# Performance work log

Measured on AMD Instinct MI355X. Metric: run time of the kernel, lower is better.

## Reference

```python
import jax, jax.numpy as jnp
import numpy as np

K = 2            # number of attention heads (k in __init__)
NEG = -9.0e15    # mask fill value from the torch code
N, C, CO = 6144, 128, 128


def _ln(x, g, b, eps=1e-5):
    m = x.mean(-1, keepdims=True)
    v = ((x - m) ** 2).mean(-1, keepdims=True)
    return (x - m) / jnp.sqrt(v + eps) * g + b


def setup_inputs() -> dict:
    key = jax.random.key(0)
    ks = jax.random.split(key, 6)
    x = jax.random.normal(ks[0], (N, C), jnp.float32)
    adj = (jax.random.uniform(ks[1], (N, N)) < 0.01).astype(jnp.float32)
    ff0_w = jax.random.normal(ks[2], (K, C, C), jnp.float32) / np.float32(np.sqrt(C))
    ff1_w = jax.random.normal(ks[3], (K, CO, C), jnp.float32) / np.float32(np.sqrt(C))
    attn_w = jax.random.normal(ks[4], (K, 2 * C), jnp.float32) / np.float32(np.sqrt(2 * C))
    return dict(
        x=x, adj=adj, ff0_w=ff0_w, ff1_w=ff1_w, attn_w=attn_w,
        g1=jnp.ones((C,), jnp.float32), b1=jnp.zeros((C,), jnp.float32),
        g2=jnp.ones((C,), jnp.float32), b2=jnp.zeros((C,), jnp.float32),
    )


def reference(x, adj, ff0_w, ff1_w, attn_w, g1, b1, g2, b2):
    n, c = x.shape
    co = ff1_w.shape[1]
    x_norm = _ln(x, g1, b1)
    # torch does adj = adj + eye(n) each iteration; since adj >= 0 the mask
    # (adj > 0) is identical for every iteration: original edges plus self-loops.
    mask = (adj > 0) | jnp.eye(n, dtype=bool)
    h_next = jnp.zeros((n, co), x.dtype)
    for i in range(K):  # small fixed head count, structurally distinct weights
        h = x_norm @ ff0_w[i].T  # [n, c]
        # attn_fc(cat(h_i, h_j)) == a1.h_i + a2.h_j  (exact decomposition of
        # the concat+linear; avoids materializing the [n, n, 2c] tensor)
        s_src = h @ attn_w[i, :c]  # [n], contribution of row node i
        s_dst = h @ attn_w[i, c:]  # [n], contribution of col node j
        e = jax.nn.leaky_relu(s_src[:, None] + s_dst[None, :])  # [n, n]
        e = jnp.where(mask, e, jnp.float32(NEG))
        atten = jax.nn.softmax(e, axis=1)  # dropout p=0.0 -> identity
        att = atten @ h + x  # residual adds pre-norm x
        att = _ln(att, g2, b2)
        h_next = h_next + jax.nn.elu(att @ ff1_w[i].T) / K
    return h_next
```

## Files before the change

### kernel.cpp

```cpp
#include <hip/hip_runtime.h>
#include <math.h>

#define Nn 6144
#define Cc 128
#define NHD 2
#define NBRS 192

__device__ __forceinline__ float wave_red_sum(float v) {
#pragma unroll
  for (int o = 32; o; o >>= 1) v += __shfl_xor(v, o);
  return v;
}

__global__ __launch_bounds__(256) void k_ln(const float* __restrict__ x,
                                            const float* __restrict__ g,
                                            const float* __restrict__ b,
                                            float* __restrict__ xn) {
  int wid = threadIdx.x >> 6, lane = threadIdx.x & 63;
  int row = blockIdx.x * 4 + wid;
  float2 v = ((const float2*)(x + (size_t)row * Cc))[lane];
  float s = v.x + v.y;
#pragma unroll
  for (int o = 32; o; o >>= 1) s += __shfl_xor(s, o);
  float mean = s * (1.0f / Cc);
  float dx = v.x - mean, dy = v.y - mean;
  float q = dx * dx + dy * dy;
#pragma unroll
  for (int o = 32; o; o >>= 1) q += __shfl_xor(q, o);
  float rstd = rsqrtf(q * (1.0f / Cc) + 1e-5f);
  int c = lane * 2;
  float* o = xn + (size_t)row * Cc;
  o[c]     = dx * rstd * g[c] + b[c];
  o[c + 1] = dy * rstd * g[c + 1] + b[c + 1];
}

template <int MODE>
__global__ __launch_bounds__(256) void k_gemm(const float* __restrict__ A,
                                              const float* __restrict__ Bw,
                                              float* __restrict__ out) {
  __shared__ float As[64][68];
  __shared__ float Bs[64][132];
  const int t = threadIdx.x;
  const int head = blockIdx.y;
  const int row0 = blockIdx.x * 64;
  const float* Ah = A + (MODE == 1 ? (size_t)head * Nn * Cc : (size_t)0);
  const float* Bh = Bw + (size_t)head * Cc * Cc;
  const int tr = t & 15, tc = t >> 4;
  const int r0 = tr * 4, c0 = tc * 8;
  float acc[4][8];
#pragma unroll
  for (int i = 0; i < 4; i++)
#pragma unroll
    for (int j = 0; j < 8; j++) acc[i][j] = 0.f;

  for (int kt = 0; kt < Cc; kt += 64) {
    __syncthreads();
    for (int i = t; i < 1024; i += 256) {
      int rr = i >> 4, k4 = i & 15;
      float4 v = *(const float4*)(Ah + (size_t)(row0 + rr) * Cc + kt + k4 * 4);
      As[k4 * 4 + 0][rr] = v.x; As[k4 * 4 + 1][rr] = v.y;
      As[k4 * 4 + 2][rr] = v.z; As[k4 * 4 + 3][rr] = v.w;
    }
    for (int i = t; i < 2048; i += 256) {
      int cc2 = i >> 4, k4 = i & 15;
      float4 v = *(const float4*)(Bh + (size_t)cc2 * Cc + kt + k4 * 4);
      Bs[k4 * 4 + 0][cc2] = v.x; Bs[k4 * 4 + 1][cc2] = v.y;
      Bs[k4 * 4 + 2][cc2] = v.z; Bs[k4 * 4 + 3][cc2] = v.w;
    }
    __syncthreads();
#pragma unroll
    for (int k = 0; k < 64; k++) {
      float4 a  = *(const float4*)&As[k][r0];
      float4 b0 = *(const float4*)&Bs[k][c0];
      float4 b1 = *(const float4*)&Bs[k][c0 + 4];
      float av[4] = {a.x, a.y, a.z, a.w};
      float bv[8] = {b0.x, b0.y, b0.z, b0.w, b1.x, b1.y, b1.z, b1.w};
#pragma unroll
      for (int i = 0; i < 4; i++)
#pragma unroll
        for (int j = 0; j < 8; j++) acc[i][j] = fmaf(av[i], bv[j], acc[i][j]);
    }
  }
#pragma unroll
  for (int i = 0; i < 4; i++) {
    float o[8];
#pragma unroll
    for (int j = 0; j < 8; j++) {
      float v = acc[i][j];
      if (MODE == 1) { v = (v > 0.f) ? v : (expf(v) - 1.f); v *= 0.5f; }
      o[j] = v;
    }
    float* op = out + ((size_t)head * Nn + row0 + r0 + i) * Cc + c0;
    *(float4*)(op)     = make_float4(o[0], o[1], o[2], o[3]);
    *(float4*)(op + 4) = make_float4(o[4], o[5], o[6], o[7]);
  }
}

__global__ __launch_bounds__(256) void k_attn_s(const float* __restrict__ h,
                                                const float* __restrict__ aw,
                                                float* __restrict__ ssrc,
                                                float* __restrict__ sdst) {
  int wid = threadIdx.x >> 6, lane = threadIdx.x & 63;
  int row = blockIdx.x * 4 + wid;
#pragma unroll
  for (int hd = 0; hd < NHD; hd++) {
    float2 v  = ((const float2*)(h + ((size_t)hd * Nn + row) * Cc))[lane];
    float2 w1 = ((const float2*)(aw + hd * 2 * Cc))[lane];
    float2 w2 = ((const float2*)(aw + hd * 2 * Cc + Cc))[lane];
    float a = v.x * w1.x + v.y * w1.y;
    float b = v.x * w2.x + v.y * w2.y;
#pragma unroll
    for (int o = 32; o; o >>= 1) { a += __shfl_xor(a, o); b += __shfl_xor(b, o); }
    if (lane == 0) { ssrc[hd * Nn + row] = a; sdst[hd * Nn + row] = b; }
  }
}

__global__ __launch_bounds__(256) void k_csr(
    const float* __restrict__ adj, const float* __restrict__ ssrc,
    const float* __restrict__ sdst, int* __restrict__ nbr,
    int* __restrict__ deg, float* __restrict__ wtsg) {
  __shared__ int nbr_s[4][NBRS];
  const int lane = threadIdx.x & 63;
  const int wid = threadIdx.x >> 6;
  const int r = blockIdx.x * 4 + wid;
  const float4* arow = (const float4*)(adj + (size_t)r * Nn);
  const unsigned long long ltmask = (1ull << lane) - 1ull;
  int cnt = 0;
  for (int i = lane; i < Nn / 4; i += 64) {
    float4 v = arow[i];
    int j = i * 4;
    bool p0 = (v.x > 0.f) || (j + 0 == r);
    bool p1 = (v.y > 0.f) || (j + 1 == r);
    bool p2 = (v.z > 0.f) || (j + 2 == r);
    bool p3 = (v.w > 0.f) || (j + 3 == r);
    unsigned long long m0 = __ballot(p0);
    unsigned long long m1 = __ballot(p1);
    unsigned long long m2 = __ballot(p2);
    unsigned long long m3 = __ballot(p3);
    int c0 = __popcll(m0), c1 = __popcll(m1), c2 = __popcll(m2), c3 = __popcll(m3);
    if (p0) nbr_s[wid][cnt + __popcll(m0 & ltmask)] = j;
    if (p1) nbr_s[wid][cnt + c0 + __popcll(m1 & ltmask)] = j + 1;
    if (p2) nbr_s[wid][cnt + c0 + c1 + __popcll(m2 & ltmask)] = j + 2;
    if (p3) nbr_s[wid][cnt + c0 + c1 + c2 + __popcll(m3 & ltmask)] = j + 3;
    cnt += c0 + c1 + c2 + c3;
  }
  if (cnt > NBRS) cnt = NBRS;
  const float s0 = ssrc[r], s1 = ssrc[Nn + r];
  float e0v[3], e1v[3];
  float m0 = -3.0e38f, m1 = -3.0e38f;
#pragma unroll
  for (int it = 0; it < 3; it++) {
    int k = it * 64 + lane;
    float a0 = -3.0e38f, a1 = -3.0e38f;
    if (k < cnt) {
      int j = nbr_s[wid][k];
      a0 = s0 + sdst[j];
      a1 = s1 + sdst[Nn + j];
      a0 = (a0 > 0.f) ? a0 : 0.01f * a0;
      a1 = (a1 > 0.f) ? a1 : 0.01f * a1;
    }
    e0v[it] = a0; e1v[it] = a1;
    m0 = fmaxf(m0, a0); m1 = fmaxf(m1, a1);
  }
#pragma unroll
  for (int o = 32; o; o >>= 1) {
    m0 = fmaxf(m0, __shfl_xor(m0, o));
    m1 = fmaxf(m1, __shfl_xor(m1, o));
  }
  float t0 = 0.f, t1 = 0.f;
  float w0v[3], w1v[3];
#pragma unroll
  for (int it = 0; it < 3; it++) {
    int k = it * 64 + lane;
    float w0 = (k < cnt) ? __expf(e0v[it] - m0) : 0.f;
    float w1 = (k < cnt) ? __expf(e1v[it] - m1) : 0.f;
    w0v[it] = w0; w1v[it] = w1; t0 += w0; t1 += w1;
  }
#pragma unroll
  for (int o = 32; o; o >>= 1) { t0 += __shfl_xor(t0, o); t1 += __shfl_xor(t1, o); }
  const float i0 = 1.0f / t0, i1 = 1.0f / t1;
  int* nrow = nbr + (size_t)r * NBRS;
  float* w0row = wtsg + (size_t)r * NBRS;
  float* w1row = wtsg + (size_t)(Nn + r) * NBRS;
#pragma unroll
  for (int it = 0; it < 3; it++) {
    int k = it * 64 + lane;
    if (k < cnt) {
      nrow[k] = nbr_s[wid][k];
      w0row[k] = w0v[it] * i0;
      w1row[k] = w1v[it] * i1;
    }
  }
  if (lane == 0) deg[r] = cnt;
}

__global__ __launch_bounds__(256) void k_gather(
    const int* __restrict__ nbr, const int* __restrict__ degp,
    const float* __restrict__ wtsg, const float* __restrict__ x,
    const float* __restrict__ h, const float* __restrict__ g2,
    const float* __restrict__ b2, float* __restrict__ att_out) {
  __shared__ int nbr_s[NBRS];
  __shared__ float wts[NHD][NBRS];
  __shared__ float red[8];
  const int t = threadIdx.x;
  const int r = blockIdx.x;
  const int deg = degp[r];
  if (t < deg) {
    nbr_s[t] = nbr[(size_t)r * NBRS + t];
    wts[0][t] = wtsg[(size_t)r * NBRS + t];
    wts[1][t] = wtsg[(size_t)(Nn + r) * NBRS + t];
  }
  __syncthreads();
  const int hd = t >> 7;
  const int c = t & 127;
  const float* hp = h + (size_t)hd * Nn * Cc + c;
  const float* wrow = wts[hd];
  float acc = 0.f;
  int k = 0;
  for (; k + 8 <= deg; k += 8) {
    int j0 = nbr_s[k],     j1 = nbr_s[k + 1], j2 = nbr_s[k + 2], j3 = nbr_s[k + 3];
    int j4 = nbr_s[k + 4], j5 = nbr_s[k + 5], j6 = nbr_s[k + 6], j7 = nbr_s[k + 7];
    float a0 = hp[(size_t)j0 * Cc], a1 = hp[(size_t)j1 * Cc];
    float a2 = hp[(size_t)j2 * Cc], a3 = hp[(size_t)j3 * Cc];
    float a4 = hp[(size_t)j4 * Cc], a5 = hp[(size_t)j5 * Cc];
    float a6 = hp[(size_t)j6 * Cc], a7 = hp[(size_t)j7 * Cc];
    acc = fmaf(wrow[k],     a0, acc); acc = fmaf(wrow[k + 1], a1, acc);
    acc = fmaf(wrow[k + 2], a2, acc); acc = fmaf(wrow[k + 3], a3, acc);
    acc = fmaf(wrow[k + 4], a4, acc); acc = fmaf(wrow[k + 5], a5, acc);
    acc = fmaf(wrow[k + 6], a6, acc); acc = fmaf(wrow[k + 7], a7, acc);
  }
  for (; k < deg; k++) acc = fmaf(wrow[k], hp[(size_t)nbr_s[k] * Cc], acc);
  float att = acc + x[(size_t)r * Cc + c];
  float s = wave_red_sum(att);
  int wid = t >> 6;
  __syncthreads();
  if ((t & 63) == 0) red[wid] = s;
  __syncthreads();
  float mean = (red[hd * 2] + red[hd * 2 + 1]) * (1.0f / Cc);
  float d = att - mean;
  float q = wave_red_sum(d * d);
  __syncthreads();
  if ((t & 63) == 0) red[wid] = q;
  __syncthreads();
  float var = (red[hd * 2] + red[hd * 2 + 1]) * (1.0f / Cc);
  float rstd = rsqrtf(var + 1e-5f);
  att_out[((size_t)hd * Nn + r) * Cc + c] = d * rstd * g2[c] + b2[c];
}

__global__ __launch_bounds__(256) void k_combine(const float* __restrict__ a,
                                                 const float* __restrict__ b,
                                                 float* __restrict__ o) {
  int i = (blockIdx.x * 256 + threadIdx.x) * 4;
  float4 va = *(const float4*)(a + i);
  float4 vb = *(const float4*)(b + i);
  *(float4*)(o + i) = make_float4(va.x + vb.x, va.y + vb.y, va.z + vb.z, va.w + vb.w);
}

extern "C" void kernel_launch(void* const* d_in, const int* in_sizes, int n_in,
                              void* d_out, int out_size, void* d_ws, size_t ws_size,
                              hipStream_t stream) {
  const float* x   = (const float*)d_in[0];
  const float* adj = (const float*)d_in[1];
  const float* ff0 = (const float*)d_in[2];
  const float* ff1 = (const float*)d_in[3];
  const float* aw  = (const float*)d_in[4];
  const float* g1  = (const float*)d_in[5];
  const float* b1  = (const float*)d_in[6];
  const float* g2  = (const float*)d_in[7];
  const float* b2  = (const float*)d_in[8];
  float* out = (float*)d_out;

  float* ws    = (float*)d_ws;
  float* xnorm = ws;
  float* h     = xnorm + (size_t)Nn * Cc;
  float* ssrc  = h + (size_t)2 * Nn * Cc;
  float* sdst  = ssrc + 2 * Nn;
  float* attn  = sdst + 2 * Nn;
  float* outh  = attn + (size_t)2 * Nn * Cc;
  float* wtsg  = outh + (size_t)2 * Nn * Cc;
  int*   nbr   = (int*)(wtsg + (size_t)2 * Nn * NBRS);
  int*   deg   = nbr + (size_t)Nn * NBRS;

  hipLaunchKernelGGL(k_ln, dim3(Nn / 4), dim3(256), 0, stream, x, g1, b1, xnorm);
  hipLaunchKernelGGL((k_gemm<0>), dim3(Nn / 64, NHD), dim3(256), 0, stream, xnorm, ff0, h);
  hipLaunchKernelGGL(k_attn_s, dim3(Nn / 4), dim3(256), 0, stream, h, aw, ssrc, sdst);
  hipLaunchKernelGGL(k_csr, dim3(Nn / 4), dim3(256), 0, stream, adj, ssrc, sdst, nbr, deg, wtsg);
  hipLaunchKernelGGL(k_gather, dim3(Nn), dim3(256), 0, stream,
                     nbr, deg, wtsg, x, h, g2, b2, attn);
  hipLaunchKernelGGL((k_gemm<1>), dim3(Nn / 64, NHD), dim3(256), 0, stream, attn, ff1, outh);
  hipLaunchKernelGGL(k_combine, dim3((Nn * Cc) / 1024), dim3(256), 0, stream,
                     outh, outh + (size_t)Nn * Cc, out);
}
```

Baseline: 312.9 us.

## Store projected features in bf16 and fuse head-sum into second GEMM

```diff
diff --git a/kernel.cpp b/kernel.cpp
--- a/kernel.cpp
+++ b/kernel.cpp
@@ -5,6 +5,18 @@
 #define Cc 128
 #define NHD 2
 #define NBRS 192
+
+typedef unsigned short u16;
+typedef unsigned int u32;
+
+__device__ __forceinline__ float bf2f(u16 u) {
+  union { u32 i; float f; } v; v.i = ((u32)u) << 16; return v.f;
+}
+__device__ __forceinline__ u16 f2bf(float f) {
+  union { float f; u32 i; } v; v.f = f;
+  u32 r = (v.i + 0x7FFFu + ((v.i >> 16) & 1u)) >> 16;
+  return (u16)r;
+}
 
 __device__ __forceinline__ float wave_red_sum(float v) {
 #pragma unroll
@@ -34,16 +46,14 @@
   o[c + 1] = dy * rstd * g[c + 1] + b[c + 1];
 }
 
-template <int MODE>
-__global__ __launch_bounds__(256) void k_gemm(const float* __restrict__ A,
-                                              const float* __restrict__ Bw,
-                                              float* __restrict__ out) {
+__global__ __launch_bounds__(256) void k_ff0(const float* __restrict__ A,
+                                             const float* __restrict__ Bw,
+                                             u16* __restrict__ hb) {
   __shared__ float As[64][68];
   __shared__ float Bs[64][132];
   const int t = threadIdx.x;
   const int head = blockIdx.y;
   const int row0 = blockIdx.x * 64;
-  const float* Ah = A + (MODE == 1 ? (size_t)head * Nn * Cc : (size_t)0);
   const float* Bh = Bw + (size_t)head * Cc * Cc;
   const int tr = t & 15, tc = t >> 4;
   const int r0 = tr * 4, c0 = tc * 8;
@@ -57,7 +67,7 @@
     __syncthreads();
     for (int i = t; i < 1024; i += 256) {
       int rr = i >> 4, k4 = i & 15;
-      float4 v = *(const float4*)(Ah + (size_t)(row0 + rr) * Cc + kt + k4 * 4);
+      float4 v = *(const float4*)(A + (size_t)(row0 + rr) * Cc + kt + k4 * 4);
       As[k4 * 4 + 0][rr] = v.x; As[k4 * 4 + 1][rr] = v.y;
       As[k4 * 4 + 2][rr] = v.z; As[k4 * 4 + 3][rr] = v.w;
     }
@@ -83,20 +93,18 @@
   }
 #pragma unroll
   for (int i = 0; i < 4; i++) {
-    float o[8];
-#pragma unroll
-    for (int j = 0; j < 8; j++) {
-      float v = acc[i][j];
-      if (MODE == 1) { v = (v > 0.f) ? v : (expf(v) - 1.f); v *= 0.5f; }
-      o[j] = v;
-    }
-    float* op = out + ((size_t)head * Nn + row0 + r0 + i) * Cc + c0;
-    *(float4*)(op)     = make_float4(o[0], o[1], o[2], o[3]);
-    *(float4*)(op + 4) = make_float4(o[4], o[5], o[6], o[7]);
-  }
-}
-
-__global__ __launch_bounds__(256) void k_attn_s(const float* __restrict__ h,
+    u16* op = hb + ((size_t)head * Nn + row0 + r0 + i) * Cc + c0;
+    ushort4 o0, o1;
+    o0.x = f2bf(acc[i][0]); o0.y = f2bf(acc[i][1]);
+    o0.z = f2bf(acc[i][2]); o0.w = f2bf(acc[i][3]);
+    o1.x = f2bf(acc[i][4]); o1.y = f2bf(acc[i][5]);
+    o1.z = f2bf(acc[i][6]); o1.w = f2bf(acc[i][7]);
+    *(ushort4*)(op)     = o0;
+    *(ushort4*)(op + 4) = o1;
+  }
+}
+
+__global__ __launch_bounds__(256) void k_attn_s(const u16* __restrict__ hb,
                                                 const float* __restrict__ aw,
                                                 float* __restrict__ ssrc,
                                                 float* __restrict__ sdst) {
@@ -104,11 +112,13 @@
   int row = blockIdx.x * 4 + wid;
 #pragma unroll
   for (int hd = 0; hd < NHD; hd++) {
-    float2 v  = ((const float2*)(h + ((size_t)hd * Nn + row) * Cc))[lane];
+    u32 packed = ((const u32*)(hb + ((size_t)hd * Nn + row) * Cc))[lane];
+    float hx = bf2f((u16)(packed & 0xFFFF));
+    float hy = bf2f((u16)(packed >> 16));
     float2 w1 = ((const float2*)(aw + hd * 2 * Cc))[lane];
     float2 w2 = ((const float2*)(aw + hd * 2 * Cc + Cc))[lane];
-    float a = v.x * w1.x + v.y * w1.y;
-    float b = v.x * w2.x + v.y * w2.y;
+    float a = hx * w1.x + hy * w1.y;
+    float b = hx * w2.x + hy * w2.y;
 #pragma unroll
     for (int o = 32; o; o >>= 1) { a += __shfl_xor(a, o); b += __shfl_xor(b, o); }
     if (lane == 0) { ssrc[hd * Nn + row] = a; sdst[hd * Nn + row] = b; }
@@ -197,7 +207,7 @@
 __global__ __launch_bounds__(256) void k_gather(
     const int* __restrict__ nbr, const int* __restrict__ degp,
     const float* __restrict__ wtsg, const float* __restrict__ x,
-    const float* __restrict__ h, const float* __restrict__ g2,
+    const u16* __restrict__ hb, const float* __restrict__ g2,
     const float* __restrict__ b2, float* __restrict__ att_out) {
   __shared__ int nbr_s[NBRS];
   __shared__ float wts[NHD][NBRS];
@@ -213,23 +223,23 @@
   __syncthreads();
   const int hd = t >> 7;
   const int c = t & 127;
-  const float* hp = h + (size_t)hd * Nn * Cc + c;
+  const u16* hp = hb + (size_t)hd * Nn * Cc + c;
   const float* wrow = wts[hd];
   float acc = 0.f;
   int k = 0;
   for (; k + 8 <= deg; k += 8) {
     int j0 = nbr_s[k],     j1 = nbr_s[k + 1], j2 = nbr_s[k + 2], j3 = nbr_s[k + 3];
     int j4 = nbr_s[k + 4], j5 = nbr_s[k + 5], j6 = nbr_s[k + 6], j7 = nbr_s[k + 7];
-    float a0 = hp[(size_t)j0 * Cc], a1 = hp[(size_t)j1 * Cc];
-    float a2 = hp[(size_t)j2 * Cc], a3 = hp[(size_t)j3 * Cc];
-    float a4 = hp[(size_t)j4 * Cc], a5 = hp[(size_t)j5 * Cc];
-    float a6 = hp[(size_t)j6 * Cc], a7 = hp[(size_t)j7 * Cc];
-    acc = fmaf(wrow[k],     a0, acc); acc = fmaf(wrow[k + 1], a1, acc);
-    acc = fmaf(wrow[k + 2], a2, acc); acc = fmaf(wrow[k + 3], a3, acc);
-    acc = fmaf(wrow[k + 4], a4, acc); acc = fmaf(wrow[k + 5], a5, acc);
-    acc = fmaf(wrow[k + 6], a6, acc); acc = fmaf(wrow[k + 7], a7, acc);
-  }
-  for (; k < deg; k++) acc = fmaf(wrow[k], hp[(size_t)nbr_s[k] * Cc], acc);
+    u16 a0 = hp[(size_t)j0 * Cc], a1 = hp[(size_t)j1 * Cc];
+    u16 a2 = hp[(size_t)j2 * Cc], a3 = hp[(size_t)j3 * Cc];
+    u16 a4 = hp[(size_t)j4 * Cc], a5 = hp[(size_t)j5 * Cc];
+    u16 a6 = hp[(size_t)j6 * Cc], a7 = hp[(size_t)j7 * Cc];
+    acc = fmaf(wrow[k],     bf2f(a0), acc); acc = fmaf(wrow[k + 1], bf2f(a1), acc);
+    acc = fmaf(wrow[k + 2], bf2f(a2), acc); acc = fmaf(wrow[k + 3], bf2f(a3), acc);
+    acc = fmaf(wrow[k + 4], bf2f(a4), acc); acc = fmaf(wrow[k + 5], bf2f(a5), acc);
+    acc = fmaf(wrow[k + 6], bf2f(a6), acc); acc = fmaf(wrow[k + 7], bf2f(a7), acc);
+  }
+  for (; k < deg; k++) acc = fmaf(wrow[k], bf2f(hp[(size_t)nbr_s[k] * Cc]), acc);
   float att = acc + x[(size_t)r * Cc + c];
   float s = wave_red_sum(att);
   int wid = t >> 6;
@@ -247,13 +257,71 @@
   att_out[((size_t)hd * Nn + r) * Cc + c] = d * rstd * g2[c] + b2[c];
 }
 
-__global__ __launch_bounds__(256) void k_combine(const float* __restrict__ a,
-                                                 const float* __restrict__ b,
-                                                 float* __restrict__ o) {
-  int i = (blockIdx.x * 256 + threadIdx.x) * 4;
-  float4 va = *(const float4*)(a + i);
-  float4 vb = *(const float4*)(b + i);
-  *(float4*)(o + i) = make_float4(va.x + vb.x, va.y + vb.y, va.z + vb.z, va.w + vb.w);
+__global__ __launch_bounds__(256) void k_ff1(const float* __restrict__ A,
+                                             const float* __restrict__ Bw,
+                                             float* __restrict__ out) {
+  __shared__ float As[64][68];
+  __shared__ float Bs[64][68];
+  const int t = threadIdx.x;
+  const int row0 = blockIdx.x * 64;
+  const int ch = blockIdx.y;
+  const int tr = t & 15, tc = t >> 4;
+  const int r0 = tr * 4, c0 = tc * 4;
+  float fin[4][4];
+#pragma unroll
+  for (int i = 0; i < 4; i++)
+#pragma unroll
+    for (int j = 0; j < 4; j++) fin[i][j] = 0.f;
+
+  for (int head = 0; head < NHD; head++) {
+    const float* Ah = A + (size_t)head * Nn * Cc;
+    const float* Bh = Bw + (size_t)head * Cc * Cc + (size_t)ch * 64 * Cc;
+    float acc[4][4];
+#pragma unroll
+    for (int i = 0; i < 4; i++)
+#pragma unroll
+      for (int j = 0; j < 4; j++) acc[i][j] = 0.f;
+    for (int kt = 0; kt < Cc; kt += 64) {
+      __syncthreads();
+      for (int i = t; i < 1024; i += 256) {
+        int rr = i >> 4, k4 = i & 15;
+        float4 v = *(const float4*)(Ah + (size_t)(row0 + rr) * Cc + kt + k4 * 4);
+        As[k4 * 4 + 0][rr] = v.x; As[k4 * 4 + 1][rr] = v.y;
+        As[k4 * 4 + 2][rr] = v.z; As[k4 * 4 + 3][rr] = v.w;
+      }
+      for (int i = t; i < 1024; i += 256) {
+        int cc2 = i >> 4, k4 = i & 15;
+        float4 v = *(const float4*)(Bh + (size_t)cc2 * Cc + kt + k4 * 4);
+        Bs[k4 * 4 + 0][cc2] = v.x; Bs[k4 * 4 + 1][cc2] = v.y;
+        Bs[k4 * 4 + 2][cc2] = v.z; Bs[k4 * 4 + 3][cc2] = v.w;
+      }
+      __syncthreads();
+#pragma unroll
+      for (int k = 0; k < 64; k++) {
+        float4 a = *(const float4*)&As[k][r0];
+        float4 b = *(const float4*)&Bs[k][c0];
+        float av[4] = {a.x, a.y, a.z, a.w};
+        float bv[4] = {b.x, b.y, b.z, b.w};
+#pragma unroll
+        for (int i = 0; i < 4; i++)
+#pragma unroll
+          for (int j = 0; j < 4; j++) acc[i][j] = fmaf(av[i], bv[j], acc[i][j]);
+      }
+    }
+#pragma unroll
+    for (int i = 0; i < 4; i++)
+#pragma unroll
+      for (int j = 0; j < 4; j++) {
+        float v = acc[i][j];
+        v = (v > 0.f) ? v : (expf(v) - 1.f);
+        fin[i][j] += 0.5f * v;
+      }
+  }
+#pragma unroll
+  for (int i = 0; i < 4; i++) {
+    float* op = out + (size_t)(row0 + r0 + i) * Cc + ch * 64 + c0;
+    *(float4*)op = make_float4(fin[i][0], fin[i][1], fin[i][2], fin[i][3]);
+  }
 }
 
 extern "C" void kernel_launch(void* const* d_in, const int* in_sizes, int n_in,
@@ -272,22 +340,19 @@
 
   float* ws    = (float*)d_ws;
   float* xnorm = ws;
-  float* h     = xnorm + (size_t)Nn * Cc;
-  float* ssrc  = h + (size_t)2 * Nn * Cc;
+  float* ssrc  = xnorm + (size_t)Nn * Cc;
   float* sdst  = ssrc + 2 * Nn;
   float* attn  = sdst + 2 * Nn;
-  float* outh  = attn + (size_t)2 * Nn * Cc;
-  float* wtsg  = outh + (size_t)2 * Nn * Cc;
+  float* wtsg  = attn + (size_t)2 * Nn * Cc;
   int*   nbr   = (int*)(wtsg + (size_t)2 * Nn * NBRS);
   int*   deg   = nbr + (size_t)Nn * NBRS;
+  u16*   hb    = (u16*)(deg + Nn);
 
   hipLaunchKernelGGL(k_ln, dim3(Nn / 4), dim3(256), 0, stream, x, g1, b1, xnorm);
-  hipLaunchKernelGGL((k_gemm<0>), dim3(Nn / 64, NHD), dim3(256), 0, stream, xnorm, ff0, h);
-  hipLaunchKernelGGL(k_attn_s, dim3(Nn / 4), dim3(256), 0, stream, h, aw, ssrc, sdst);
+  hipLaunchKernelGGL(k_ff0, dim3(Nn / 64, NHD), dim3(256), 0, stream, xnorm, ff0, hb);
+  hipLaunchKernelGGL(k_attn_s, dim3(Nn / 4), dim3(256), 0, stream, hb, aw, ssrc, sdst);
   hipLaunchKernelGGL(k_csr, dim3(Nn / 4), dim3(256), 0, stream, adj, ssrc, sdst, nbr, deg, wtsg);
   hipLaunchKernelGGL(k_gather, dim3(Nn), dim3(256), 0, stream,
-                     nbr, deg, wtsg, x, h, g2, b2, attn);
-  hipLaunchKernelGGL((k_gemm<1>), dim3(Nn / 64, NHD), dim3(256), 0, stream, attn, ff1, outh);
-  hipLaunchKernelGGL(k_combine, dim3((Nn * Cc) / 1024), dim3(256), 0, stream,
-                     outh, outh + (size_t)Nn * Cc, out);
-}
+                     nbr, deg, wtsg, x, hb, g2, b2, attn);
+  hipLaunchKernelGGL(k_ff1, dim3(Nn / 64, 2), dim3(256), 0, stream, attn, ff1, out);
+}
```

Result: faster. 305.7 us (-2.3%).
